# Optimization experiments

Hardware: AMD Instinct MI355X
Metric: run time of the kernel (lower is better)

## Reference

```python
import jax, jax.numpy as jnp
import numpy as np

N_NODES = 20000
N_EDGES = 640000
IN_DIM = 128
HID = 128
OUT_DIM = 3
N_GRAPHS = 32


def setup_inputs() -> dict:
    key = jax.random.key(0)
    ks = jax.random.split(key, 12)
    x = jax.random.normal(ks[0], (N_NODES, IN_DIM), dtype=jnp.float32)
    edge_index = jax.random.randint(ks[1], (2, N_EDGES), 0, N_NODES, dtype=jnp.int64)
    batch = jnp.sort(jax.random.randint(ks[2], (N_NODES,), 0, N_GRAPHS, dtype=jnp.int64))
    batch = batch.at[0].set(0).at[-1].set(N_GRAPHS - 1)
    s = 0.05
    W_gcn = jax.random.normal(ks[3], (IN_DIM, HID), jnp.float32) * s
    b_gcn = jnp.zeros((HID,), jnp.float32)
    W_sage_l = jax.random.normal(ks[4], (HID, HID), jnp.float32) * s  # neighbor branch
    W_sage_r = jax.random.normal(ks[5], (HID, HID), jnp.float32) * s  # root branch
    b_sage = jnp.zeros((HID,), jnp.float32)
    W_fc1 = jax.random.normal(ks[6], (HID, HID), jnp.float32) * s
    b_fc1 = jnp.zeros((HID,), jnp.float32)
    W_fc2 = jax.random.normal(ks[7], (HID, OUT_DIM), jnp.float32) * s
    b_fc2 = jnp.zeros((OUT_DIM,), jnp.float32)
    return {
        'x': x, 'edge_index': edge_index, 'batch': batch,
        'W_gcn': W_gcn, 'b_gcn': b_gcn,
        'W_sage_l': W_sage_l, 'W_sage_r': W_sage_r, 'b_sage': b_sage,
        'W_fc1': W_fc1, 'b_fc1': b_fc1, 'W_fc2': W_fc2, 'b_fc2': b_fc2,
    }


def reference(x, edge_index, batch, W_gcn, b_gcn, W_sage_l, W_sage_r, b_sage,
              W_fc1, b_fc1, W_fc2, b_fc2):
    n = x.shape[0]
    row, col = edge_index[0], edge_index[1]  # source -> target

    # ---- GCNConv: symmetric-normalized aggregation with self-loops ----
    h = x @ W_gcn  # [N, H]
    loops = jnp.arange(n, dtype=row.dtype)
    row_sl = jnp.concatenate([row, loops])
    col_sl = jnp.concatenate([col, loops])
    deg = jax.ops.segment_sum(jnp.ones_like(col_sl, dtype=h.dtype), col_sl,
                              num_segments=n)
    dinv = jnp.where(deg > 0, jax.lax.rsqrt(deg), 0.0)
    norm = dinv[row_sl] * dinv[col_sl]  # [E+N]
    h_gcn = jax.ops.segment_sum(h[row_sl] * norm[:, None], col_sl,
                                num_segments=n) + b_gcn
    h_gcn = jax.nn.relu(h_gcn)

    # ---- SAGEConv (mean aggregator) ----
    cnt = jax.ops.segment_sum(jnp.ones_like(col, dtype=h_gcn.dtype), col,
                              num_segments=n)
    neigh = jax.ops.segment_sum(h_gcn[row], col, num_segments=n)
    neigh = neigh / jnp.maximum(cnt, 1.0)[:, None]
    h_sage = neigh @ W_sage_l + h_gcn @ W_sage_r + b_sage
    h_sage = jax.nn.relu(h_sage)

    # ---- global_add_pool (num_graphs = 32 < 50) ----
    pooled = jax.ops.segment_sum(h_sage, batch, num_segments=N_GRAPHS)  # [G, H]

    # ---- MLP head ----
    out = jax.nn.relu(pooled @ W_fc1 + b_fc1) @ W_fc2 + b_fc2  # [G, 3]
    return out
```

## Files before the change

kernel.cpp:

```cpp
#include <hip/hip_runtime.h>

#define N_NODES 20000
#define N_EDGES 640000
#define HID 128
#define N_GRAPHS 32

#define SCAN_BLK 256
#define SCAN_NBLK ((N_NODES + SCAN_BLK - 1) / SCAN_BLK)

#define XT_STRIDE 36

__global__ __launch_bounds__(256) void hist_k(const int* __restrict__ col,
                                              int* __restrict__ cnt) {
    int e = blockIdx.x * blockDim.x + threadIdx.x;
    if (e < N_EDGES) {
        int c = col[e];
        if ((unsigned)c < N_NODES) atomicAdd(&cnt[c], 1);
    }
}

__global__ __launch_bounds__(SCAN_BLK) void scanA_k(const int* __restrict__ cnt,
                                                    int* __restrict__ blkSum) {
    __shared__ int wsum[SCAN_BLK / 64];
    const int b = blockIdx.x, t = threadIdx.x;
    const int i = b * SCAN_BLK + t;
    int v = (i < N_NODES) ? cnt[i] : 0;
#pragma unroll
    for (int o = 1; o < 64; o <<= 1) v += __shfl_xor(v, o);
    if ((t & 63) == 0) wsum[t >> 6] = v;
    __syncthreads();
    if (t == 0) {
        int s = 0;
#pragma unroll
        for (int w = 0; w < SCAN_BLK / 64; ++w) s += wsum[w];
        blkSum[b] = s;
    }
}

__global__ __launch_bounds__(SCAN_BLK) void scanB_k(const int* __restrict__ cnt,
                                                    const int* __restrict__ blkSum,
                                                    int* __restrict__ offs,
                                                    int* __restrict__ cursor,
                                                    float* __restrict__ dinv,
                                                    float* __restrict__ pooled) {
    __shared__ int sm[SCAN_BLK];
    __shared__ int base_s;
    const int b = blockIdx.x, t = threadIdx.x;
    const int i = b * SCAN_BLK + t;
    const int v = (i < N_NODES) ? cnt[i] : 0;
    sm[t] = v;
    if (b == 0) {
#pragma unroll
        for (int j = 0; j < (N_GRAPHS * HID) / SCAN_BLK; ++j)
            pooled[j * SCAN_BLK + t] = 0.f;
    }
    if (t == 0) {
        int s = 0;
        for (int k = 0; k < b; ++k) s += blkSum[k];
        base_s = s;
    }
    __syncthreads();
    for (int o = 1; o < SCAN_BLK; o <<= 1) {
        int add = (t >= o) ? sm[t - o] : 0;
        __syncthreads();
        sm[t] += add;
        __syncthreads();
    }
    if (i < N_NODES) {
        int excl = base_s + ((t > 0) ? sm[t - 1] : 0);
        offs[i] = excl;
        cursor[i] = excl;
        dinv[i] = rsqrtf((float)(v + 1));
        if (i == N_NODES - 1) offs[N_NODES] = excl + v;
    }
}

__global__ __launch_bounds__(256) void fill_k(const int* __restrict__ row,
                                              const int* __restrict__ col,
                                              int* __restrict__ cursor,
                                              int* __restrict__ csr_src) {
    int e = blockIdx.x * blockDim.x + threadIdx.x;
    if (e < N_EDGES) {
        int c = col[e];
        int r = row[e];
        if ((unsigned)c < N_NODES && (unsigned)r < N_NODES) {
            int p = atomicAdd(&cursor[c], 1);
            csr_src[p] = r;
        }
    }
}

__device__ __forceinline__ void stage_xt(float* xt, const float* __restrict__ Xm,
                                         int row0, int t) {
    const int r = t & 31;
    const int kbase = (t >> 5) * 16;
    const float* xp = Xm + (size_t)(row0 + r) * 128 + kbase;
#pragma unroll
    for (int c = 0; c < 4; ++c) {
        float4 v = *(const float4*)&xp[c * 4];
        xt[(kbase + c * 4 + 0) * XT_STRIDE + r] = v.x;
        xt[(kbase + c * 4 + 1) * XT_STRIDE + r] = v.y;
        xt[(kbase + c * 4 + 2) * XT_STRIDE + r] = v.z;
        xt[(kbase + c * 4 + 3) * XT_STRIDE + r] = v.w;
    }
}

__device__ __forceinline__ void gemm_half(const float* xt, const float* wbuf,
                                          int kb, int rg, int c4, float4 acc[4]) {
#pragma unroll 8
    for (int k0 = 0; k0 < 64; ++k0) {
        float4 w = *(const float4*)&wbuf[k0 * 128 + c4];
        float4 xr = *(const float4*)&xt[(kb + k0) * XT_STRIDE + rg * 4];
        acc[0].x = fmaf(xr.x, w.x, acc[0].x);
        acc[0].y = fmaf(xr.x, w.y, acc[0].y);
        acc[0].z = fmaf(xr.x, w.z, acc[0].z);
        acc[0].w = fmaf(xr.x, w.w, acc[0].w);
        acc[1].x = fmaf(xr.y, w.x, acc[1].x);
        acc[1].y = fmaf(xr.y, w.y, acc[1].y);
        acc[1].z = fmaf(xr.y, w.z, acc[1].z);
        acc[1].w = fmaf(xr.y, w.w, acc[1].w);
        acc[2].x = fmaf(xr.z, w.x, acc[2].x);
        acc[2].y = fmaf(xr.z, w.y, acc[2].y);
        acc[2].z = fmaf(xr.z, w.z, acc[2].z);
        acc[2].w = fmaf(xr.z, w.w, acc[2].w);
        acc[3].x = fmaf(xr.w, w.x, acc[3].x);
        acc[3].y = fmaf(xr.w, w.y, acc[3].y);
        acc[3].z = fmaf(xr.w, w.z, acc[3].z);
        acc[3].w = fmaf(xr.w, w.w, acc[3].w);
    }
}

__global__ __launch_bounds__(256) void gemm128_k(const float* __restrict__ X,
                                                 const float* __restrict__ W,
                                                 float* __restrict__ Y) {
    __shared__ float wbuf[64 * 128];
    __shared__ float xt[128 * XT_STRIDE];
    const int t = threadIdx.x;
    const int rg = t >> 5;
    const int c4 = (t & 31) * 4;
    const int row0 = blockIdx.x * 32;
    float4 acc[4];
    acc[0] = acc[1] = acc[2] = acc[3] = make_float4(0.f, 0.f, 0.f, 0.f);
    stage_xt(xt, X, row0, t);
#pragma unroll
    for (int kc = 0; kc < 2; ++kc) {
        if (kc) __syncthreads();
#pragma unroll
        for (int i = 0; i < 8; ++i)
            ((float4*)wbuf)[t + i * 256] = ((const float4*)W)[kc * 2048 + t + i * 256];
        __syncthreads();
        gemm_half(xt, wbuf, kc * 64, rg, c4, acc);
    }
#pragma unroll
    for (int i = 0; i < 4; ++i)
        *(float4*)&Y[(size_t)(row0 + rg * 4 + i) * 128 + c4] = acc[i];
}

__global__ __launch_bounds__(256) void gcn_agg_k(const float* __restrict__ h,
                                                 const int* __restrict__ offs,
                                                 const int* __restrict__ src,
                                                 const float* __restrict__ dinv,
                                                 const float* __restrict__ bias,
                                                 float* __restrict__ out) {
    const int wave = threadIdx.x >> 6;
    const int lane = threadIdx.x & 63;
    const int half = lane >> 5;
    const int node = (blockIdx.x * 4 + wave) * 2 + half;
    const int c4 = (lane & 31) * 4;
    const int nd = (node < N_NODES) ? node : (N_NODES - 1);
    const float dc = dinv[nd];
    float4 hv = *(const float4*)&h[(size_t)nd * 128 + c4];
    float4 acc = make_float4(dc * hv.x, dc * hv.y, dc * hv.z, dc * hv.w);
    const int beg = offs[nd];
    const int deg = offs[nd + 1] - beg;
    const int mdeg = max(deg, __shfl(deg, lane ^ 32));
    for (int j = 0; j < mdeg; j += 4) {
        int i0 = (j + 0 < deg) ? beg + j + 0 : 0;
        int i1 = (j + 1 < deg) ? beg + j + 1 : 0;
        int i2 = (j + 2 < deg) ? beg + j + 2 : 0;
        int i3 = (j + 3 < deg) ? beg + j + 3 : 0;
        int s0 = src[i0], s1 = src[i1], s2 = src[i2], s3 = src[i3];
        float w0 = (j + 0 < deg) ? dinv[s0] : 0.f;
        float w1 = (j + 1 < deg) ? dinv[s1] : 0.f;
        float w2 = (j + 2 < deg) ? dinv[s2] : 0.f;
        float w3 = (j + 3 < deg) ? dinv[s3] : 0.f;
        float4 v0 = *(const float4*)&h[(size_t)s0 * 128 + c4];
        float4 v1 = *(const float4*)&h[(size_t)s1 * 128 + c4];
        float4 v2 = *(const float4*)&h[(size_t)s2 * 128 + c4];
        float4 v3 = *(const float4*)&h[(size_t)s3 * 128 + c4];
        acc.x = fmaf(w0, v0.x, fmaf(w1, v1.x, fmaf(w2, v2.x, fmaf(w3, v3.x, acc.x))));
        acc.y = fmaf(w0, v0.y, fmaf(w1, v1.y, fmaf(w2, v2.y, fmaf(w3, v3.y, acc.y))));
        acc.z = fmaf(w0, v0.z, fmaf(w1, v1.z, fmaf(w2, v2.z, fmaf(w3, v3.z, acc.z))));
        acc.w = fmaf(w0, v0.w, fmaf(w1, v1.w, fmaf(w2, v2.w, fmaf(w3, v3.w, acc.w))));
    }
    float4 b = *(const float4*)&bias[c4];
    float4 o;
    o.x = fmaxf(fmaf(dc, acc.x, b.x), 0.f);
    o.y = fmaxf(fmaf(dc, acc.y, b.y), 0.f);
    o.z = fmaxf(fmaf(dc, acc.z, b.z), 0.f);
    o.w = fmaxf(fmaf(dc, acc.w, b.w), 0.f);
    if (node < N_NODES) *(float4*)&out[(size_t)node * 128 + c4] = o;
}

__global__ __launch_bounds__(256) void fused_sc_k(const float* __restrict__ hg,
                                                  const int* __restrict__ offs,
                                                  const int* __restrict__ src,
                                                  const float* __restrict__ Wl,
                                                  const float* __restrict__ Wr,
                                                  const float* __restrict__ bias,
                                                  float* __restrict__ Y) {
    __shared__ float wbuf[64 * 128];
    __shared__ float xt[128 * XT_STRIDE];
    const int t = threadIdx.x;
    const int wave = t >> 6;
    const int lane = t & 63;
    const int half = lane >> 5;
    const int c4 = (lane & 31) * 4;
    const int row0 = blockIdx.x * 32;
#pragma unroll
    for (int p = 0; p < 4; ++p) {
        const int nodeLocal = wave * 8 + p * 2 + half;
        const int node = row0 + nodeLocal;
        float4 acc = make_float4(0.f, 0.f, 0.f, 0.f);
        const int beg = offs[node];
        const int deg = offs[node + 1] - beg;
        const int mdeg = max(deg, __shfl(deg, lane ^ 32));
        for (int j = 0; j < mdeg; j += 4) {
            int i0 = (j + 0 < deg) ? beg + j + 0 : 0;
            int i1 = (j + 1 < deg) ? beg + j + 1 : 0;
            int i2 = (j + 2 < deg) ? beg + j + 2 : 0;
            int i3 = (j + 3 < deg) ? beg + j + 3 : 0;
            float w0 = (j + 0 < deg) ? 1.f : 0.f;
            float w1 = (j + 1 < deg) ? 1.f : 0.f;
            float w2 = (j + 2 < deg) ? 1.f : 0.f;
            float w3 = (j + 3 < deg) ? 1.f : 0.f;
            int s0 = src[i0], s1 = src[i1], s2 = src[i2], s3 = src[i3];
            float4 v0 = *(const float4*)&hg[(size_t)s0 * 128 + c4];
            float4 v1 = *(const float4*)&hg[(size_t)s1 * 128 + c4];
            float4 v2 = *(const float4*)&hg[(size_t)s2 * 128 + c4];
            float4 v3 = *(const float4*)&hg[(size_t)s3 * 128 + c4];
            acc.x = fmaf(w0, v0.x, fmaf(w1, v1.x, fmaf(w2, v2.x, fmaf(w3, v3.x, acc.x))));
            acc.y = fmaf(w0, v0.y, fmaf(w1, v1.y, fmaf(w2, v2.y, fmaf(w3, v3.y, acc.y))));
            acc.z = fmaf(w0, v0.z, fmaf(w1, v1.z, fmaf(w2, v2.z, fmaf(w3, v3.z, acc.z))));
            acc.w = fmaf(w0, v0.w, fmaf(w1, v1.w, fmaf(w2, v2.w, fmaf(w3, v3.w, acc.w))));
        }
        const float inv = 1.0f / (float)max(deg, 1);
        xt[(c4 + 0) * XT_STRIDE + nodeLocal] = acc.x * inv;
        xt[(c4 + 1) * XT_STRIDE + nodeLocal] = acc.y * inv;
        xt[(c4 + 2) * XT_STRIDE + nodeLocal] = acc.z * inv;
        xt[(c4 + 3) * XT_STRIDE + nodeLocal] = acc.w * inv;
    }
    const int rg = t >> 5;
    const int gc4 = (t & 31) * 4;
    float4 acc[4];
    {
        float4 b = *(const float4*)&bias[gc4];
        acc[0] = acc[1] = acc[2] = acc[3] = b;
    }
#pragma unroll
    for (int m = 0; m < 2; ++m) {
        const float* Wm = m ? Wr : Wl;
        if (m) {
            __syncthreads();
            stage_xt(xt, hg, row0, t);
        }
#pragma unroll
        for (int kc = 0; kc < 2; ++kc) {
            __syncthreads();
#pragma unroll
            for (int i = 0; i < 8; ++i)
                ((float4*)wbuf)[t + i * 256] = ((const float4*)Wm)[kc * 2048 + t + i * 256];
            __syncthreads();
            gemm_half(xt, wbuf, kc * 64, rg, gc4, acc);
        }
    }
#pragma unroll
    for (int i = 0; i < 4; ++i) {
        float4 o = acc[i];
        o.x = fmaxf(o.x, 0.f);
        o.y = fmaxf(o.y, 0.f);
        o.z = fmaxf(o.z, 0.f);
        o.w = fmaxf(o.w, 0.f);
        *(float4*)&Y[(size_t)(row0 + rg * 4 + i) * 128 + gc4] = o;
    }
}

#define POOL_ROWS 64
__global__ __launch_bounds__(256) void pool_k(const float* __restrict__ H,
                                              const int* __restrict__ batch,
                                              float* __restrict__ pooled) {
    const int r0 = blockIdx.x * POOL_ROWS;
    const int t = threadIdx.x;
    const int d = t & 127, half = t >> 7;
    const int rend = min(r0 + POOL_ROWS, N_NODES);
    int i = r0 + half;
    if (i >= rend) return;
    int cur = batch[i];
    float acc = 0.f;
    for (; i < rend; i += 2) {
        int g = batch[i];
        if (g != cur) {
            atomicAdd(&pooled[cur * 128 + d], acc);
            acc = 0.f;
            cur = g;
        }
        acc += H[(size_t)i * 128 + d];
    }
    atomicAdd(&pooled[cur * 128 + d], acc);
}

__global__ __launch_bounds__(128) void head_k(const float* __restrict__ pooled,
                                              const float* __restrict__ Wfc1,
                                              const float* __restrict__ bfc1,
                                              const float* __restrict__ Wfc2,
                                              const float* __restrict__ bfc2,
                                              float* __restrict__ out) {
    __shared__ float pl[128];
    __shared__ float tmp[128];
    const int g = blockIdx.x;
    const int t = threadIdx.x;
    pl[t] = pooled[g * 128 + t];
    __syncthreads();
    float a = bfc1[t];
#pragma unroll 8
    for (int k = 0; k < 128; ++k) a = fmaf(pl[k], Wfc1[k * 128 + t], a);
    tmp[t] = fmaxf(a, 0.f);
    __syncthreads();
    if (t < 3) {
        float a2 = bfc2[t];
        for (int k = 0; k < 128; ++k) a2 = fmaf(tmp[k], Wfc2[k * 3 + t], a2);
        out[g * 3 + t] = a2;
    }
}

extern "C" void kernel_launch(void* const* d_in, const int* in_sizes, int n_in,
                              void* d_out, int out_size, void* d_ws, size_t ws_size,
                              hipStream_t stream) {
    const float* x      = (const float*)d_in[0];
    const int*   ei     = (const int*)d_in[1];
    const int*   batch  = (const int*)d_in[2];
    const float* W_gcn  = (const float*)d_in[3];
    const float* b_gcn  = (const float*)d_in[4];
    const float* W_sl   = (const float*)d_in[5];
    const float* W_sr   = (const float*)d_in[6];
    const float* b_sage = (const float*)d_in[7];
    const float* W_fc1  = (const float*)d_in[8];
    const float* b_fc1  = (const float*)d_in[9];
    const float* W_fc2  = (const float*)d_in[10];
    const float* b_fc2  = (const float*)d_in[11];
    float* out = (float*)d_out;

    char* base = (char*)d_ws;
    size_t off = 0;
    auto take = [&](size_t bytes) -> void* {
        void* p = base + off;
        off += (bytes + 255) & ~(size_t)255;
        return p;
    };
    int*   cnt      = (int*)take((size_t)N_NODES * 4);
    int*   offs     = (int*)take((size_t)(N_NODES + 1) * 4);
    int*   cursor   = (int*)take((size_t)N_NODES * 4);
    float* dinv     = (float*)take((size_t)N_NODES * 4);
    int*   blkSum   = (int*)take((size_t)SCAN_NBLK * 4);
    int*   csr_src  = (int*)take((size_t)N_EDGES * 4);
    float* bufA     = (float*)take((size_t)N_NODES * HID * 4);
    float* bufB     = (float*)take((size_t)N_NODES * HID * 4);
    float* pooled   = (float*)take((size_t)N_GRAPHS * HID * 4);

    const int* row = ei;
    const int* col = ei + N_EDGES;

    hipMemsetAsync(cnt, 0, (size_t)N_NODES * 4, stream);

    hist_k<<<(N_EDGES + 255) / 256, 256, 0, stream>>>(col, cnt);
    scanA_k<<<SCAN_NBLK, SCAN_BLK, 0, stream>>>(cnt, blkSum);
    scanB_k<<<SCAN_NBLK, SCAN_BLK, 0, stream>>>(cnt, blkSum, offs, cursor, dinv, pooled);
    fill_k<<<(N_EDGES + 255) / 256, 256, 0, stream>>>(row, col, cursor, csr_src);

    const int gemm_blocks = N_NODES / 32;
    const int agg_blocks = (N_NODES + 7) / 8;
    gemm128_k<<<gemm_blocks, 256, 0, stream>>>(x, W_gcn, bufA);
    gcn_agg_k<<<agg_blocks, 256, 0, stream>>>(bufA, offs, csr_src, dinv, b_gcn, bufB);
    fused_sc_k<<<gemm_blocks, 256, 0, stream>>>(bufB, offs, csr_src, W_sl, W_sr,
                                                b_sage, bufA);
    pool_k<<<(N_NODES + POOL_ROWS - 1) / POOL_ROWS, 256, 0, stream>>>(bufA, batch, pooled);
    head_k<<<N_GRAPHS, 128, 0, stream>>>(pooled, W_fc1, b_fc1, W_fc2, b_fc2, out);
}
```

Measured before the change: 294.5 us.

## Gather with 16-lane groups over two 64-column passes and prefetch weights

The gather kernels now give each node 16 lanes instead of 32 and cover the 128 features in two passes of 64 columns. Each wave therefore handles four nodes at a time, so each 64-lane instruction spans more distinct rows and the max-degree padding is shared by fewer lanes per node. The fused SAGE kernel loads its first weight chunk to shared memory before the aggregation phase and makes the barrier sequence explicit. The cost is that the index and dinv loads are repeated in each pass, and the wave now idles on the largest of four node degrees rather than two.

```diff
diff --git a/kernel.cpp b/kernel.cpp
--- a/kernel.cpp
+++ b/kernel.cpp
@@ -103,6 +103,13 @@
         xt[(kbase + c * 4 + 2) * XT_STRIDE + r] = v.z;
         xt[(kbase + c * 4 + 3) * XT_STRIDE + r] = v.w;
     }
+}
+
+__device__ __forceinline__ void stage_w(float* wbuf, const float* __restrict__ Wm,
+                                        int kc, int t) {
+#pragma unroll
+    for (int i = 0; i < 8; ++i)
+        ((float4*)wbuf)[t + i * 256] = ((const float4*)Wm)[kc * 2048 + t + i * 256];
 }
 
 __device__ __forceinline__ void gemm_half(const float* xt, const float* wbuf,
@@ -142,15 +149,13 @@
     float4 acc[4];
     acc[0] = acc[1] = acc[2] = acc[3] = make_float4(0.f, 0.f, 0.f, 0.f);
     stage_xt(xt, X, row0, t);
-#pragma unroll
-    for (int kc = 0; kc < 2; ++kc) {
-        if (kc) __syncthreads();
-#pragma unroll
-        for (int i = 0; i < 8; ++i)
-            ((float4*)wbuf)[t + i * 256] = ((const float4*)W)[kc * 2048 + t + i * 256];
-        __syncthreads();
-        gemm_half(xt, wbuf, kc * 64, rg, c4, acc);
-    }
+    stage_w(wbuf, W, 0, t);
+    __syncthreads();
+    gemm_half(xt, wbuf, 0, rg, c4, acc);
+    __syncthreads();
+    stage_w(wbuf, W, 1, t);
+    __syncthreads();
+    gemm_half(xt, wbuf, 64, rg, c4, acc);
 #pragma unroll
     for (int i = 0; i < 4; ++i)
         *(float4*)&Y[(size_t)(row0 + rg * 4 + i) * 128 + c4] = acc[i];
@@ -164,42 +169,46 @@
                                                  float* __restrict__ out) {
     const int wave = threadIdx.x >> 6;
     const int lane = threadIdx.x & 63;
-    const int half = lane >> 5;
-    const int node = (blockIdx.x * 4 + wave) * 2 + half;
-    const int c4 = (lane & 31) * 4;
-    const int nd = (node < N_NODES) ? node : (N_NODES - 1);
-    const float dc = dinv[nd];
-    float4 hv = *(const float4*)&h[(size_t)nd * 128 + c4];
-    float4 acc = make_float4(dc * hv.x, dc * hv.y, dc * hv.z, dc * hv.w);
-    const int beg = offs[nd];
-    const int deg = offs[nd + 1] - beg;
-    const int mdeg = max(deg, __shfl(deg, lane ^ 32));
-    for (int j = 0; j < mdeg; j += 4) {
-        int i0 = (j + 0 < deg) ? beg + j + 0 : 0;
-        int i1 = (j + 1 < deg) ? beg + j + 1 : 0;
-        int i2 = (j + 2 < deg) ? beg + j + 2 : 0;
-        int i3 = (j + 3 < deg) ? beg + j + 3 : 0;
-        int s0 = src[i0], s1 = src[i1], s2 = src[i2], s3 = src[i3];
-        float w0 = (j + 0 < deg) ? dinv[s0] : 0.f;
-        float w1 = (j + 1 < deg) ? dinv[s1] : 0.f;
-        float w2 = (j + 2 < deg) ? dinv[s2] : 0.f;
-        float w3 = (j + 3 < deg) ? dinv[s3] : 0.f;
-        float4 v0 = *(const float4*)&h[(size_t)s0 * 128 + c4];
-        float4 v1 = *(const float4*)&h[(size_t)s1 * 128 + c4];
-        float4 v2 = *(const float4*)&h[(size_t)s2 * 128 + c4];
-        float4 v3 = *(const float4*)&h[(size_t)s3 * 128 + c4];
-        acc.x = fmaf(w0, v0.x, fmaf(w1, v1.x, fmaf(w2, v2.x, fmaf(w3, v3.x, acc.x))));
-        acc.y = fmaf(w0, v0.y, fmaf(w1, v1.y, fmaf(w2, v2.y, fmaf(w3, v3.y, acc.y))));
-        acc.z = fmaf(w0, v0.z, fmaf(w1, v1.z, fmaf(w2, v2.z, fmaf(w3, v3.z, acc.z))));
-        acc.w = fmaf(w0, v0.w, fmaf(w1, v1.w, fmaf(w2, v2.w, fmaf(w3, v3.w, acc.w))));
-    }
-    float4 b = *(const float4*)&bias[c4];
-    float4 o;
-    o.x = fmaxf(fmaf(dc, acc.x, b.x), 0.f);
-    o.y = fmaxf(fmaf(dc, acc.y, b.y), 0.f);
-    o.z = fmaxf(fmaf(dc, acc.z, b.z), 0.f);
-    o.w = fmaxf(fmaf(dc, acc.w, b.w), 0.f);
-    if (node < N_NODES) *(float4*)&out[(size_t)node * 128 + c4] = o;
+    const int sub = lane >> 4;
+    const int node = (blockIdx.x * 4 + wave) * 4 + sub;
+    const int c0 = (lane & 15) * 4;
+    const float dc = dinv[node];
+    const int beg = offs[node];
+    const int deg = offs[node + 1] - beg;
+    int md = max(deg, __shfl(deg, lane ^ 16));
+    md = max(md, __shfl(md, lane ^ 32));
+#pragma unroll
+    for (int pass = 0; pass < 2; ++pass) {
+        const int c4 = c0 + pass * 64;
+        float4 hv = *(const float4*)&h[(size_t)node * 128 + c4];
+        float4 acc = make_float4(dc * hv.x, dc * hv.y, dc * hv.z, dc * hv.w);
+        for (int j = 0; j < md; j += 4) {
+            int i0 = (j + 0 < deg) ? beg + j + 0 : 0;
+            int i1 = (j + 1 < deg) ? beg + j + 1 : 0;
+            int i2 = (j + 2 < deg) ? beg + j + 2 : 0;
+            int i3 = (j + 3 < deg) ? beg + j + 3 : 0;
+            int s0 = src[i0], s1 = src[i1], s2 = src[i2], s3 = src[i3];
+            float w0 = (j + 0 < deg) ? dinv[s0] : 0.f;
+            float w1 = (j + 1 < deg) ? dinv[s1] : 0.f;
+            float w2 = (j + 2 < deg) ? dinv[s2] : 0.f;
+            float w3 = (j + 3 < deg) ? dinv[s3] : 0.f;
+            float4 v0 = *(const float4*)&h[(size_t)s0 * 128 + c4];
+            float4 v1 = *(const float4*)&h[(size_t)s1 * 128 + c4];
+            float4 v2 = *(const float4*)&h[(size_t)s2 * 128 + c4];
+            float4 v3 = *(const float4*)&h[(size_t)s3 * 128 + c4];
+            acc.x = fmaf(w0, v0.x, fmaf(w1, v1.x, fmaf(w2, v2.x, fmaf(w3, v3.x, acc.x))));
+            acc.y = fmaf(w0, v0.y, fmaf(w1, v1.y, fmaf(w2, v2.y, fmaf(w3, v3.y, acc.y))));
+            acc.z = fmaf(w0, v0.z, fmaf(w1, v1.z, fmaf(w2, v2.z, fmaf(w3, v3.z, acc.z))));
+            acc.w = fmaf(w0, v0.w, fmaf(w1, v1.w, fmaf(w2, v2.w, fmaf(w3, v3.w, acc.w))));
+        }
+        float4 b = *(const float4*)&bias[c4];
+        float4 o;
+        o.x = fmaxf(fmaf(dc, acc.x, b.x), 0.f);
+        o.y = fmaxf(fmaf(dc, acc.y, b.y), 0.f);
+        o.z = fmaxf(fmaf(dc, acc.z, b.z), 0.f);
+        o.w = fmaxf(fmaf(dc, acc.w, b.w), 0.f);
+        *(float4*)&out[(size_t)node * 128 + c4] = o;
+    }
 }
 
 __global__ __launch_bounds__(256) void fused_sc_k(const float* __restrict__ hg,
@@ -214,42 +223,49 @@
     const int t = threadIdx.x;
     const int wave = t >> 6;
     const int lane = t & 63;
-    const int half = lane >> 5;
-    const int c4 = (lane & 31) * 4;
+    const int sub = lane >> 4;
+    const int c0 = (lane & 15) * 4;
     const int row0 = blockIdx.x * 32;
-#pragma unroll
-    for (int p = 0; p < 4; ++p) {
-        const int nodeLocal = wave * 8 + p * 2 + half;
-        const int node = row0 + nodeLocal;
-        float4 acc = make_float4(0.f, 0.f, 0.f, 0.f);
-        const int beg = offs[node];
-        const int deg = offs[node + 1] - beg;
-        const int mdeg = max(deg, __shfl(deg, lane ^ 32));
-        for (int j = 0; j < mdeg; j += 4) {
-            int i0 = (j + 0 < deg) ? beg + j + 0 : 0;
-            int i1 = (j + 1 < deg) ? beg + j + 1 : 0;
-            int i2 = (j + 2 < deg) ? beg + j + 2 : 0;
-            int i3 = (j + 3 < deg) ? beg + j + 3 : 0;
-            float w0 = (j + 0 < deg) ? 1.f : 0.f;
-            float w1 = (j + 1 < deg) ? 1.f : 0.f;
-            float w2 = (j + 2 < deg) ? 1.f : 0.f;
-            float w3 = (j + 3 < deg) ? 1.f : 0.f;
-            int s0 = src[i0], s1 = src[i1], s2 = src[i2], s3 = src[i3];
-            float4 v0 = *(const float4*)&hg[(size_t)s0 * 128 + c4];
-            float4 v1 = *(const float4*)&hg[(size_t)s1 * 128 + c4];
-            float4 v2 = *(const float4*)&hg[(size_t)s2 * 128 + c4];
-            float4 v3 = *(const float4*)&hg[(size_t)s3 * 128 + c4];
-            acc.x = fmaf(w0, v0.x, fmaf(w1, v1.x, fmaf(w2, v2.x, fmaf(w3, v3.x, acc.x))));
-            acc.y = fmaf(w0, v0.y, fmaf(w1, v1.y, fmaf(w2, v2.y, fmaf(w3, v3.y, acc.y))));
-            acc.z = fmaf(w0, v0.z, fmaf(w1, v1.z, fmaf(w2, v2.z, fmaf(w3, v3.z, acc.z))));
-            acc.w = fmaf(w0, v0.w, fmaf(w1, v1.w, fmaf(w2, v2.w, fmaf(w3, v3.w, acc.w))));
+    stage_w(wbuf, Wl, 0, t);
+#pragma unroll
+    for (int pass = 0; pass < 2; ++pass) {
+        const int c4 = c0 + pass * 64;
+#pragma unroll
+        for (int p = 0; p < 2; ++p) {
+            const int nodeLocal = p * 16 + wave * 4 + sub;
+            const int node = row0 + nodeLocal;
+            float4 acc = make_float4(0.f, 0.f, 0.f, 0.f);
+            const int beg = offs[node];
+            const int deg = offs[node + 1] - beg;
+            int md = max(deg, __shfl(deg, lane ^ 16));
+            md = max(md, __shfl(md, lane ^ 32));
+            for (int j = 0; j < md; j += 4) {
+                int i0 = (j + 0 < deg) ? beg + j + 0 : 0;
+                int i1 = (j + 1 < deg) ? beg + j + 1 : 0;
+                int i2 = (j + 2 < deg) ? beg + j + 2 : 0;
+                int i3 = (j + 3 < deg) ? beg + j + 3 : 0;
+                float w0 = (j + 0 < deg) ? 1.f : 0.f;
+                float w1 = (j + 1 < deg) ? 1.f : 0.f;
+                float w2 = (j + 2 < deg) ? 1.f : 0.f;
+                float w3 = (j + 3 < deg) ? 1.f : 0.f;
+                int s0 = src[i0], s1 = src[i1], s2 = src[i2], s3 = src[i3];
+                float4 v0 = *(const float4*)&hg[(size_t)s0 * 128 + c4];
+                float4 v1 = *(const float4*)&hg[(size_t)s1 * 128 + c4];
+                float4 v2 = *(const float4*)&hg[(size_t)s2 * 128 + c4];
+                float4 v3 = *(const float4*)&hg[(size_t)s3 * 128 + c4];
+                acc.x = fmaf(w0, v0.x, fmaf(w1, v1.x, fmaf(w2, v2.x, fmaf(w3, v3.x, acc.x))));
+                acc.y = fmaf(w0, v0.y, fmaf(w1, v1.y, fmaf(w2, v2.y, fmaf(w3, v3.y, acc.y))));
+                acc.z = fmaf(w0, v0.z, fmaf(w1, v1.z, fmaf(w2, v2.z, fmaf(w3, v3.z, acc.z))));
+                acc.w = fmaf(w0, v0.w, fmaf(w1, v1.w, fmaf(w2, v2.w, fmaf(w3, v3.w, acc.w))));
+            }
+            const float inv = 1.0f / (float)max(deg, 1);
+            xt[(c4 + 0) * XT_STRIDE + nodeLocal] = acc.x * inv;
+            xt[(c4 + 1) * XT_STRIDE + nodeLocal] = acc.y * inv;
+            xt[(c4 + 2) * XT_STRIDE + nodeLocal] = acc.z * inv;
+            xt[(c4 + 3) * XT_STRIDE + nodeLocal] = acc.w * inv;
         }
-        const float inv = 1.0f / (float)max(deg, 1);
-        xt[(c4 + 0) * XT_STRIDE + nodeLocal] = acc.x * inv;
-        xt[(c4 + 1) * XT_STRIDE + nodeLocal] = acc.y * inv;
-        xt[(c4 + 2) * XT_STRIDE + nodeLocal] = acc.z * inv;
-        xt[(c4 + 3) * XT_STRIDE + nodeLocal] = acc.w * inv;
-    }
+    }
+    __syncthreads();
     const int rg = t >> 5;
     const int gc4 = (t & 31) * 4;
     float4 acc[4];
@@ -257,23 +273,20 @@
         float4 b = *(const float4*)&bias[gc4];
         acc[0] = acc[1] = acc[2] = acc[3] = b;
     }
-#pragma unroll
-    for (int m = 0; m < 2; ++m) {
-        const float* Wm = m ? Wr : Wl;
-        if (m) {
-            __syncthreads();
-            stage_xt(xt, hg, row0, t);
-        }
-#pragma unroll
-        for (int kc = 0; kc < 2; ++kc) {
-            __syncthreads();
-#pragma unroll
-            for (int i = 0; i < 8; ++i)
-                ((float4*)wbuf)[t + i * 256] = ((const float4*)Wm)[kc * 2048 + t + i * 256];
-            __syncthreads();
-            gemm_half(xt, wbuf, kc * 64, rg, gc4, acc);
-        }
-    }
+    gemm_half(xt, wbuf, 0, rg, gc4, acc);
+    __syncthreads();
+    stage_w(wbuf, Wl, 1, t);
+    __syncthreads();
+    gemm_half(xt, wbuf, 64, rg, gc4, acc);
+    __syncthreads();
+    stage_xt(xt, hg, row0, t);
+    stage_w(wbuf, Wr, 0, t);
+    __syncthreads();
+    gemm_half(xt, wbuf, 0, rg, gc4, acc);
+    __syncthreads();
+    stage_w(wbuf, Wr, 1, t);
+    __syncthreads();
+    gemm_half(xt, wbuf, 64, rg, gc4, acc);
 #pragma unroll
     for (int i = 0; i < 4; ++i) {
         float4 o = acc[i];
@@ -378,7 +391,7 @@
     fill_k<<<(N_EDGES + 255) / 256, 256, 0, stream>>>(row, col, cursor, csr_src);
 
     const int gemm_blocks = N_NODES / 32;
-    const int agg_blocks = (N_NODES + 7) / 8;
+    const int agg_blocks  = N_NODES / 16;
     gemm128_k<<<gemm_blocks, 256, 0, stream>>>(x, W_gcn, bufA);
     gcn_agg_k<<<agg_blocks, 256, 0, stream>>>(bufA, offs, csr_src, dinv, b_gcn, bufB);
     fused_sc_k<<<gemm_blocks, 256, 0, stream>>>(bufB, offs, csr_src, W_sl, W_sr,
```

After: 292.2 us. Within noise of the previous version (-0.8%).
